# Kernel optimization log

Measured on AMD Instinct MI355X. Metric: run time of the kernel, lower is better.

The kernel has to match this reference:

```python
import jax, jax.numpy as jnp
import numpy as np

B, S, N, D = 8, 2048, 512, 1024
MAX_W = 32  # fixed max span width (inclusive widths 0..MAX_W-1)
MASK_FILL = -1000.0


def setup_inputs() -> dict:
    key = jax.random.key(0)
    k1, k2, k3, k4 = jax.random.split(key, 4)
    sequence_tensor = jax.random.normal(k1, (B, S, D), dtype=jnp.float32)
    starts = jax.random.randint(k2, (B, N), 0, S - MAX_W)
    widths = jax.random.randint(k3, (B, N), 0, MAX_W)  # inclusive width = widths
    span_indices = jnp.stack([starts, starts + widths], axis=-1)  # (B, N, 2)
    att_w = jax.random.normal(k4, (D, 1), dtype=jnp.float32) * 0.02
    att_b = jnp.zeros((1,), dtype=jnp.float32)
    return {"sequence_tensor": sequence_tensor, "span_indices": span_indices,
            "att_w": att_w, "att_b": att_b}


def reference(sequence_tensor, span_indices, att_w, att_b):
    dtype = sequence_tensor.dtype
    starts = span_indices[..., 0]               # (B, N)
    ends = span_indices[..., 1]                 # (B, N), inclusive
    widths = ends - starts                      # (B, N)

    rng = jnp.arange(MAX_W)                     # (W,)
    raw_idx = ends[..., None] - rng             # (B, N, W), walks backward from end
    span_mask = (rng <= widths[..., None]) & (raw_idx >= 0)  # (B, N, W)
    idx = jnp.maximum(raw_idx, 0)               # relu on indices

    # global attention logits: (B, S, 1)
    logits = sequence_tensor @ att_w + att_b

    b, n = idx.shape[0], idx.shape[1]
    flat = idx.reshape(b, n * MAX_W)            # (B, N*W)
    # gather embeddings and logits over the time axis
    span_emb = jnp.take_along_axis(sequence_tensor, flat[..., None], axis=1)
    span_emb = span_emb.reshape(b, n, MAX_W, -1)              # (B, N, W, D)
    span_logits = jnp.take_along_axis(logits[..., 0], flat, axis=1)
    span_logits = span_logits.reshape(b, n, MAX_W)            # (B, N, W)

    # memory-efficient masked softmax: fill masked logits with -1000
    masked_logits = jnp.where(span_mask, span_logits, jnp.asarray(MASK_FILL, dtype))
    attn = jax.nn.softmax(masked_logits, axis=-1)             # (B, N, W)

    # weighted-sum pooling over span positions
    return jnp.einsum('bnw,bnwd->bnd', attn, span_emb)
```

## Files before the change

kernel.cpp:

```cpp
#include <hip/hip_runtime.h>

#define B 8
#define S 2048
#define N 512
#define D 1024
#define MAX_W 32
#define MASK_FILL -1000.0f

typedef float vfloat4 __attribute__((ext_vector_type(4)));
typedef __fp16 half2v __attribute__((ext_vector_type(2)));
typedef unsigned int uint;

__device__ inline uint pack_f16x2(float x, float y) {
#if __has_builtin(__builtin_amdgcn_cvt_pkrtz)
    half2v r = __builtin_amdgcn_cvt_pkrtz(x, y);
    return __builtin_bit_cast(uint, r);
#else
    half2v r; r[0] = (__fp16)x; r[1] = (__fp16)y;
    return __builtin_bit_cast(uint, r);
#endif
}

__device__ inline float dot2(uint a, uint b, float c) {
    half2v x = __builtin_bit_cast(half2v, a);
    half2v y = __builtin_bit_cast(half2v, b);
#if __has_builtin(__builtin_amdgcn_fdot2)
    return __builtin_amdgcn_fdot2(x, y, c, false);
#else
    return c + (float)x[0] * (float)y[0] + (float)x[1] * (float)y[1];
#endif
}

__global__ __launch_bounds__(512) void prep_kernel(
    const float* __restrict__ seq,
    const float* __restrict__ att_w,
    const float* __restrict__ att_b,
    float* __restrict__ logits,
    unsigned short* __restrict__ seqh)
{
    const int row  = blockIdx.x * 8 + (threadIdx.x >> 6);
    const int lane = threadIdx.x & 63;

    const float4* rp = (const float4*)(seq + (size_t)row * D);
    const float4* wp = (const float4*)att_w;

    float4 a[4];
    float acc = 0.0f;
#pragma unroll
    for (int k = 0; k < 4; ++k) {
        a[k] = rp[lane + 64 * k];
        const float4 w = wp[lane + 64 * k];
        acc += a[k].x * w.x + a[k].y * w.y + a[k].z * w.z + a[k].w * w.w;
    }

    uint2* hp = (uint2*)(seqh + (size_t)row * D);
#pragma unroll
    for (int k = 0; k < 4; ++k) {
        uint2 h;
        h.x = pack_f16x2(a[k].x, a[k].y);
        h.y = pack_f16x2(a[k].z, a[k].w);
        hp[lane + 64 * k] = h;
    }

#pragma unroll
    for (int off = 32; off > 0; off >>= 1)
        acc += __shfl_down(acc, off);
    if (lane == 0)
        logits[row] = acc + att_b[0];
}

__global__ __launch_bounds__(256) void pool_kernel(
    const unsigned short* __restrict__ seqh,
    const int*   __restrict__ spans,
    const float* __restrict__ logits,
    float* __restrict__ out)
{
    const int b    = blockIdx.x & 7;
    const int n    = blockIdx.x >> 3;
    const int span = b * N + n;

    const int start = spans[2 * span + 0];
    const int end   = spans[2 * span + 1];
    const int width = end - start;

    __shared__ uint  s_ah2[MAX_W];
    __shared__ uint  s_off[MAX_W];
    __shared__ float s_part[128][9];

    const int tid  = threadIdx.x;
    const int c    = tid & 127;
    const int half = tid >> 7;

    if (tid < MAX_W) {
        const int w   = tid;
        const int raw = end - w;
        const bool valid = (w <= width) && (raw >= 0);
        const int idx = raw > start ? raw : start;
        const float l = valid ? logits[b * S + idx] : MASK_FILL;

        float m = l;
#pragma unroll
        for (int off = 16; off > 0; off >>= 1)
            m = fmaxf(m, __shfl_down(m, off, 32));
        m = __shfl(m, 0, 32);

        const float p = __expf(l - m);

        float sum = p;
#pragma unroll
        for (int off = 16; off > 0; off >>= 1)
            sum += __shfl_down(sum, off, 32);
        sum = __shfl(sum, 0, 32);

        const float at  = p / sum;
        const float at2 = __shfl_down(at, 2, 32);
        s_ah2[w] = pack_f16x2(at, at2);
        s_off[w] = (uint)idx << 11;
    }
    __syncthreads();

    const char* sb  = (const char*)seqh + (size_t)b * S * D * 2;
    const uint  cvo = (uint)c * 16u;

    float acc[8];
#pragma unroll
    for (int j = 0; j < 8; ++j) acc[j] = 0.0f;

    const int cnt  = width + 1;
    const int cnt8 = (cnt + 7) & ~7;

#define LDROW(OFF) (*(const uint4*)(sb + (OFF) + cvo))

    uint4 q0 = LDROW(s_off[half + 0]);
    uint4 q1 = LDROW(s_off[half + 2]);
    uint4 q2 = LDROW(s_off[half + 4]);
    uint4 q3 = LDROW(s_off[half + 6]);

    for (int w = 0; w < cnt8; w += 8) {
        const uint aA = s_ah2[w + half + 0];
        const uint aB = s_ah2[w + half + 4];

        uint4 n0, n1, n2, n3;
        const bool more = (w + 8) < cnt8;
        if (more) {
            const int v0 = w + 8 + half;
            n0 = LDROW(s_off[v0 + 0]);
            n1 = LDROW(s_off[v0 + 2]);
            n2 = LDROW(s_off[v0 + 4]);
            n3 = LDROW(s_off[v0 + 6]);
        }

#define PAIR(qx, qy, ah, jlo, jhi)                                          \
        acc[jlo] = dot2(ah, __builtin_amdgcn_perm(qy, qx, 0x05040100u),     \
                        acc[jlo]);                                          \
        acc[jhi] = dot2(ah, __builtin_amdgcn_perm(qy, qx, 0x07060302u),     \
                        acc[jhi]);

        PAIR(q0.x, q1.x, aA, 0, 1)
        PAIR(q0.y, q1.y, aA, 2, 3)
        PAIR(q0.z, q1.z, aA, 4, 5)
        PAIR(q0.w, q1.w, aA, 6, 7)
        PAIR(q2.x, q3.x, aB, 0, 1)
        PAIR(q2.y, q3.y, aB, 2, 3)
        PAIR(q2.z, q3.z, aB, 4, 5)
        PAIR(q2.w, q3.w, aB, 6, 7)
#undef PAIR

        if (more) { q0 = n0; q1 = n1; q2 = n2; q3 = n3; }
    }
#undef LDROW

    if (half == 1) {
#pragma unroll
        for (int j = 0; j < 8; ++j) s_part[c][j] = acc[j];
    }
    __syncthreads();
    if (half == 0) {
#pragma unroll
        for (int j = 0; j < 8; ++j) acc[j] += s_part[c][j];

        vfloat4 va;
        va.x = acc[0]; va.y = acc[1]; va.z = acc[2]; va.w = acc[3];
        vfloat4* op = ((vfloat4*)(out + (size_t)span * D)) + 2 * c;
        __builtin_nontemporal_store(va, op);
        va.x = acc[4]; va.y = acc[5]; va.z = acc[6]; va.w = acc[7];
        __builtin_nontemporal_store(va, op + 1);
    }
}

extern "C" void kernel_launch(void* const* d_in, const int* in_sizes, int n_in,
                              void* d_out, int out_size, void* d_ws, size_t ws_size,
                              hipStream_t stream)
{
    const float* seq    = (const float*)d_in[0];
    const int*   spans  = (const int*)  d_in[1];
    const float* att_w  = (const float*)d_in[2];
    const float* att_b  = (const float*)d_in[3];

    float* out    = (float*)d_out;
    float* logits = (float*)d_ws;
    unsigned short* seqh =
        (unsigned short*)((char*)d_ws + (size_t)B * S * sizeof(float));

    prep_kernel<<<(B * S) / 8, 512, 0, stream>>>(seq, att_w, att_b,
                                                 logits, seqh);
    pool_kernel<<<B * N, 256, 0, stream>>>(seqh, spans, logits, out);
}
```

Baseline: 117.0 us.

## Assign one wavefront per span in pool kernel, removing shared memory and barriers

The pooling kernel now maps each 64-lane wavefront to one span (four spans per block) instead of a 256-thread block per span. Softmax weights and row offsets stay in registers and are broadcast with shuffles, which removes the shared-memory staging, both __syncthreads, and the cross-half reduction. Each lane now covers 16 output channels and the loop walks only the needed position pairs rather than padding to multiples of 8. This cuts per-position padding work and block overhead, in exchange for more registers per thread and fewer memory loads in flight per span.

```diff
diff --git a/kernel.cpp b/kernel.cpp
--- a/kernel.cpp
+++ b/kernel.cpp
@@ -76,116 +76,102 @@
     float* __restrict__ out)
 {
     const int b    = blockIdx.x & 7;
-    const int n    = blockIdx.x >> 3;
+    const int wid  = threadIdx.x >> 6;
+    const int n    = (blockIdx.x >> 3) * 4 + wid;
     const int span = b * N + n;
+    const int lane = threadIdx.x & 63;
 
     const int start = spans[2 * span + 0];
     const int end   = spans[2 * span + 1];
     const int width = end - start;
 
-    __shared__ uint  s_ah2[MAX_W];
-    __shared__ uint  s_off[MAX_W];
-    __shared__ float s_part[128][9];
+    const int  w     = lane;
+    const int  raw   = end - w;
+    const bool valid = (w <= width) && (raw >= 0);
+    const int idx = raw > start ? raw : start;
+    const float l = valid ? logits[b * S + idx] : MASK_FILL;
 
-    const int tid  = threadIdx.x;
-    const int c    = tid & 127;
-    const int half = tid >> 7;
+    float m = l;
+#pragma unroll
+    for (int off = 16; off > 0; off >>= 1)
+        m = fmaxf(m, __shfl_down(m, off, 32));
+    m = __shfl(m, 0, 32);
 
-    if (tid < MAX_W) {
-        const int w   = tid;
-        const int raw = end - w;
-        const bool valid = (w <= width) && (raw >= 0);
-        const int idx = raw > start ? raw : start;
-        const float l = valid ? logits[b * S + idx] : MASK_FILL;
+    const float p = __expf(l - m);
 
-        float m = l;
+    float sum = p;
 #pragma unroll
-        for (int off = 16; off > 0; off >>= 1)
-            m = fmaxf(m, __shfl_down(m, off, 32));
-        m = __shfl(m, 0, 32);
+    for (int off = 16; off > 0; off >>= 1)
+        sum += __shfl_down(sum, off, 32);
+    sum = __shfl(sum, 0, 32);
 
-        const float p = __expf(l - m);
-
-        float sum = p;
-#pragma unroll
-        for (int off = 16; off > 0; off >>= 1)
-            sum += __shfl_down(sum, off, 32);
-        sum = __shfl(sum, 0, 32);
-
-        const float at  = p / sum;
-        const float at2 = __shfl_down(at, 2, 32);
-        s_ah2[w] = pack_f16x2(at, at2);
-        s_off[w] = (uint)idx << 11;
-    }
-    __syncthreads();
+    const float at = p / sum;
+    const uint ah2  = pack_f16x2(at, __shfl_down(at, 1, 32));
+    const uint offr = (uint)idx << 11;
 
     const char* sb  = (const char*)seqh + (size_t)b * S * D * 2;
-    const uint  cvo = (uint)c * 16u;
+    const uint  cvo = (uint)lane * 16u;
 
-    float acc[8];
+    float acc[16];
 #pragma unroll
-    for (int j = 0; j < 8; ++j) acc[j] = 0.0f;
+    for (int j = 0; j < 16; ++j) acc[j] = 0.0f;
 
-    const int cnt  = width + 1;
-    const int cnt8 = (cnt + 7) & ~7;
+    const int cnt   = width + 1;
+    const int pairs = (cnt + 1) >> 1;
 
-#define LDROW(OFF) (*(const uint4*)(sb + (OFF) + cvo))
+#define LDROW(OFF, ADD) (*(const uint4*)(sb + (OFF) + cvo + (ADD)))
 
-    uint4 q0 = LDROW(s_off[half + 0]);
-    uint4 q1 = LDROW(s_off[half + 2]);
-    uint4 q2 = LDROW(s_off[half + 4]);
-    uint4 q3 = LDROW(s_off[half + 6]);
+    uint o0 = __shfl(offr, 0);
+    uint o1 = __shfl(offr, 1);
+    uint4 qa0 = LDROW(o0, 0);
+    uint4 qb0 = LDROW(o0, 1024);
+    uint4 qa1 = LDROW(o1, 0);
+    uint4 qb1 = LDROW(o1, 1024);
 
-    for (int w = 0; w < cnt8; w += 8) {
-        const uint aA = s_ah2[w + half + 0];
-        const uint aB = s_ah2[w + half + 4];
+    for (int pp = 0; pp < pairs; ++pp) {
+        const uint ah = __shfl(ah2, 2 * pp);
 
-        uint4 n0, n1, n2, n3;
-        const bool more = (w + 8) < cnt8;
+        uint4 na0, nb0, na1, nb1;
+        const bool more = (pp + 1) < pairs;
         if (more) {
-            const int v0 = w + 8 + half;
-            n0 = LDROW(s_off[v0 + 0]);
-            n1 = LDROW(s_off[v0 + 2]);
-            n2 = LDROW(s_off[v0 + 4]);
-            n3 = LDROW(s_off[v0 + 6]);
+            const uint m0 = __shfl(offr, 2 * pp + 2);
+            const uint m1 = __shfl(offr, 2 * pp + 3);
+            na0 = LDROW(m0, 0);
+            nb0 = LDROW(m0, 1024);
+            na1 = LDROW(m1, 0);
+            nb1 = LDROW(m1, 1024);
         }
 
-#define PAIR(qx, qy, ah, jlo, jhi)                                          \
+#define PAIR(qx, qy, jlo, jhi)                                              \
         acc[jlo] = dot2(ah, __builtin_amdgcn_perm(qy, qx, 0x05040100u),     \
                         acc[jlo]);                                          \
         acc[jhi] = dot2(ah, __builtin_amdgcn_perm(qy, qx, 0x07060302u),     \
                         acc[jhi]);
 
-        PAIR(q0.x, q1.x, aA, 0, 1)
-        PAIR(q0.y, q1.y, aA, 2, 3)
-        PAIR(q0.z, q1.z, aA, 4, 5)
-        PAIR(q0.w, q1.w, aA, 6, 7)
-        PAIR(q2.x, q3.x, aB, 0, 1)
-        PAIR(q2.y, q3.y, aB, 2, 3)
-        PAIR(q2.z, q3.z, aB, 4, 5)
-        PAIR(q2.w, q3.w, aB, 6, 7)
+        PAIR(qa0.x, qa1.x,  0,  1)
+        PAIR(qa0.y, qa1.y,  2,  3)
+        PAIR(qa0.z, qa1.z,  4,  5)
+        PAIR(qa0.w, qa1.w,  6,  7)
+        PAIR(qb0.x, qb1.x,  8,  9)
+        PAIR(qb0.y, qb1.y, 10, 11)
+        PAIR(qb0.z, qb1.z, 12, 13)
+        PAIR(qb0.w, qb1.w, 14, 15)
 #undef PAIR
 
-        if (more) { q0 = n0; q1 = n1; q2 = n2; q3 = n3; }
+        if (more) { qa0 = na0; qb0 = nb0; qa1 = na1; qb1 = nb1; }
     }
 #undef LDROW
 
-    if (half == 1) {
-#pragma unroll
-        for (int j = 0; j < 8; ++j) s_part[c][j] = acc[j];
-    }
-    __syncthreads();
-    if (half == 0) {
-#pragma unroll
-        for (int j = 0; j < 8; ++j) acc[j] += s_part[c][j];
-
-        vfloat4 va;
-        va.x = acc[0]; va.y = acc[1]; va.z = acc[2]; va.w = acc[3];
-        vfloat4* op = ((vfloat4*)(out + (size_t)span * D)) + 2 * c;
-        __builtin_nontemporal_store(va, op);
-        va.x = acc[4]; va.y = acc[5]; va.z = acc[6]; va.w = acc[7];
-        __builtin_nontemporal_store(va, op + 1);
-    }
+    float* orow = out + (size_t)span * D;
+    vfloat4 v;
+    v.x = acc[0];  v.y = acc[1];  v.z = acc[2];  v.w = acc[3];
+    __builtin_nontemporal_store(v, (vfloat4*)(orow + 8 * lane));
+    v.x = acc[4];  v.y = acc[5];  v.z = acc[6];  v.w = acc[7];
+    __builtin_nontemporal_store(v, (vfloat4*)(orow + 8 * lane + 4));
+    v.x = acc[8];  v.y = acc[9];  v.z = acc[10]; v.w = acc[11];
+    __builtin_nontemporal_store(v, (vfloat4*)(orow + 512 + 8 * lane));
+    v.x = acc[12]; v.y = acc[13]; v.z = acc[14]; v.w = acc[15];
+    __builtin_nontemporal_store(v, (vfloat4*)(orow + 512 + 8 * lane + 4));
 }
 
 extern "C" void kernel_launch(void* const* d_in, const int* in_sizes, int n_in,
@@ -204,5 +190,5 @@
 
     prep_kernel<<<(B * S) / 8, 512, 0, stream>>>(seq, att_w, att_b,
                                                  logits, seqh);
-    pool_kernel<<<B * N, 256, 0, stream>>>(seqh, spans, logits, out);
+    pool_kernel<<<(B * N) / 4, 256, 0, stream>>>(seqh, spans, logits, out);
 }
```

Measured after the change: 117.9 us. Within noise of the previous version (+0.8%).
